# Kernel tuning notes

Measured on AMD Instinct MI355X. Metric: run time of the kernel, lower is better.

## Reference

```python
import jax, jax.numpy as jnp
import numpy as np

DIM = 192
T, H, W = 6, 8, 8
NH = 6
HD = DIM // NH
HW = H * W
N = T * HW
SCALE = HD ** (-0.5)
B_ = 128


def _sine_pos_enc():
    # Faithful port of get_sine_position_encoding(window_size[1:], dim // 2).
    npf = DIM // 2
    ones = jnp.ones((1, H, W), jnp.float32)
    y_embed = jnp.cumsum(ones, axis=1)
    x_embed = jnp.cumsum(ones, axis=2)
    two_pi = 2.0 * np.pi
    y_embed = y_embed / (y_embed[:, -1:, :] + 1e-6) * two_pi
    x_embed = x_embed / (x_embed[:, :, -1:] + 1e-6) * two_pi
    dim_t = jnp.arange(npf, dtype=jnp.float32)
    dim_t = 10000.0 ** (2.0 * jnp.floor(dim_t / 2.0) / npf)
    pos_x = x_embed[:, :, :, None] / dim_t
    pos_y = y_embed[:, :, :, None] / dim_t
    pos_x = jnp.stack((jnp.sin(pos_x[..., 0::2]), jnp.cos(pos_x[..., 1::2])), axis=4).reshape(1, H, W, npf)
    pos_y = jnp.stack((jnp.sin(pos_y[..., 0::2]), jnp.cos(pos_y[..., 1::2])), axis=4).reshape(1, H, W, npf)
    pos = jnp.concatenate((pos_y, pos_x), axis=3)  # (1, H, W, DIM)
    return pos.reshape(1, HW, DIM)


def setup_inputs() -> dict:
    key = jax.random.key(0)
    ks = jax.random.split(key, 6)
    s = 0.02
    return {
        "x": jax.random.normal(ks[0], (B_, N, DIM), jnp.float32),
        "Wqkv": jax.random.normal(ks[1], (3 * DIM, DIM), jnp.float32) * s,
        "Wproj": jax.random.normal(ks[2], (DIM, 2 * DIM), jnp.float32) * s,
        "bproj": jnp.zeros((DIM,), jnp.float32),
        "gamma": jnp.ones((DIM,), jnp.float32),
        "beta": jnp.zeros((DIM,), jnp.float32),
        "W1": jax.random.normal(ks[3], (DIM, DIM), jnp.float32) * s,
        "b1": jnp.zeros((DIM,), jnp.float32),
        "W2": jax.random.normal(ks[4], (DIM, DIM), jnp.float32) * s,
        "b2": jnp.zeros((DIM,), jnp.float32),
    }


def reference(x, Wqkv, Wproj, bproj, gamma, beta, W1, b1, W2, b2):
    b = x.shape[0]
    pos = jnp.tile(_sine_pos_enc(), (1, T, 1))  # (1, N, DIM)
    qkv = (x + pos) @ Wqkv.T                      # (b, N, 3*DIM)
    qkv = qkv.reshape(b, N, 3, NH, HD).transpose(2, 0, 3, 1, 4)
    # temporal chunks: (b, NH, T, HW, HD)
    q = qkv[0].reshape(b, NH, T, HW, HD)
    k = qkv[1].reshape(b, NH, T, HW, HD)
    v = qkv[2].reshape(b, NH, T, HW, HD)
    # all T x T cross-frame attention pairs at once
    scores = jnp.einsum('bhind,bhjmd->ijbhnm', q * SCALE, k)  # (T,T,b,NH,HW,HW)
    attn = jax.nn.softmax(scores, axis=-1)
    o = jnp.einsum('ijbhnm,bhjmd->ijbnhd', attn, v).reshape(T, T, b, HW, DIM)
    # Faithful to torch's x.view(-1, B_, HW, C): raw reinterpretation, not a transpose.
    x_tmp = x.reshape(T, b, HW, DIM)
    xi = jnp.broadcast_to(x_tmp[:, None], (T, T, b, HW, DIM))
    x_att = jnp.concatenate((o, xi), axis=-1)     # (T,T,b,HW,2*DIM)
    y = x_att @ Wproj.T + bproj
    mu = jnp.mean(y, axis=-1, keepdims=True)
    var = jnp.var(y, axis=-1, keepdims=True)
    y = (y - mu) / jnp.sqrt(var + 1e-5) * gamma + beta
    y = jax.nn.gelu(y @ W1.T + b1, approximate=False) @ W2.T + b2
    acc = jnp.sum(y, axis=1)                       # sum over j -> (T,b,HW,DIM)
    x_out = x + acc.transpose(1, 0, 2, 3).reshape(b, N, DIM) / T
    return jnp.concatenate((x, x_out), axis=-1)
```

## Files before the change

kernel.cpp:

```cpp
#include <hip/hip_runtime.h>
#include <cmath>

#define TT   6
#define NB   128
#define DIM  192
#define SCALE 0.17677669529663687f

typedef __attribute__((ext_vector_type(8))) short v8s;
typedef __attribute__((ext_vector_type(4))) float v4f;

__device__ __forceinline__ short f2bf(float f) {
  union { float f; unsigned u; } v; v.f = f;
  unsigned r = v.u + 0x7fffu + ((v.u >> 16) & 1u);
  return (short)(r >> 16);
}

__global__ void prep_kernel(const float* __restrict__ Wqkv, const float* __restrict__ Wproj,
                            const float* __restrict__ W1, const float* __restrict__ W2,
                            short* __restrict__ dWqkv, short* __restrict__ dWproj,
                            short* __restrict__ dW1, short* __restrict__ dW2,
                            float* __restrict__ pos) {
  int idx = blockIdx.x * 256 + threadIdx.x;
  const float* src = nullptr; short* dst = nullptr; int off = 0;
  if (idx < 27648)      { src = Wqkv;  dst = dWqkv;  off = idx; }
  else if (idx < 46080) { src = Wproj; dst = dWproj; off = idx - 27648; }
  else if (idx < 55296) { src = W1;    dst = dW1;    off = idx - 46080; }
  else if (idx < 64512) { src = W2;    dst = dW2;    off = idx - 55296; }
  else if (idx < 67584) {
    int p0 = (idx - 64512) * 4;
    float4 r;
    float* rp = (float*)&r;
#pragma unroll
    for (int jj = 0; jj < 4; jj++) {
      int p = p0 + jj;
      int row = p / 192, c = p - row * 192;
      int e  = (c < 96) ? (row >> 3) : (row & 7);
      int cc = (c < 96) ? c : c - 96;
      int m = cc >> 1;
      float embed = (float)(e + 1) * (6.283185307179586f / 8.000001f);
      float dt = powf(10000.0f, (float)m * (1.0f / 48.0f));
      float ang = embed / dt;
      rp[jj] = (cc & 1) ? cosf(ang) : sinf(ang);
    }
    *(float4*)(pos + p0) = r;
    return;
  } else return;
  const float* s = src + off * 4;
  short4 r;
  r.x = f2bf(s[0]); r.y = f2bf(s[1]); r.z = f2bf(s[2]); r.w = f2bf(s[3]);
  *(short4*)(dst + off * 4) = r;
}

__global__ __launch_bounds__(256) void qkv_kernel(
    const float* __restrict__ x, const float* __restrict__ pos,
    const short* __restrict__ Wqkv_bf,
    short* __restrict__ Qb, short* __restrict__ Kb, short* __restrict__ Vtb) {
  __shared__ short XP[64 * 200];
  int bid = blockIdx.x;
  int xcd = bid & 7, idx = bid >> 3;
  int bq = idx / TT;
  int b = xcd * 16 + bq, t = idx - bq * TT;
  int tid = threadIdx.x, w = tid >> 6, lane = tid & 63;
  int l15 = lane & 15, quad = lane >> 4;
  const float* xrow = x + (size_t)(b * (TT * 64) + t * 64) * DIM;
  for (int c = tid; c < 64 * 24; c += 256) {
    int row = c / 24, col8 = (c - (c / 24) * 24) * 8;
    const float* xs = xrow + row * DIM + col8;
    const float* pp = pos + row * DIM + col8;
    v8s r8;
#pragma unroll
    for (int jj = 0; jj < 8; jj++) r8[jj] = f2bf(xs[jj] + pp[jj]);
    *(v8s*)(XP + row * 200 + col8) = r8;
  }
  __syncthreads();
  const v4f vzero = {0.f, 0.f, 0.f, 0.f};
  size_t obase = (size_t)(b * TT + t) * 64 * DIM;
#pragma unroll
  for (int cti = 0; cti < 9; cti++) {
    int r0 = w * 144 + cti * 16;
    v4f acc[4] = {vzero, vzero, vzero, vzero};
#pragma unroll
    for (int ks = 0; ks < 6; ks++) {
      v8s a = *(const v8s*)(Wqkv_bf + (size_t)(r0 + l15) * 192 + ks * 32 + quad * 8);
#pragma unroll
      for (int nt = 0; nt < 4; nt++) {
        v8s bb = *(const v8s*)(XP + (nt * 16 + l15) * 200 + ks * 32 + quad * 8);
        acc[nt] = __builtin_amdgcn_mfma_f32_16x16x32_bf16(a, bb, acc[nt], 0, 0, 0);
      }
    }
    int R = r0 + quad * 4;
#pragma unroll
    for (int nt = 0; nt < 4; nt++) {
      int hw = nt * 16 + l15;
      if (R < 192) {
        short4 s;
        s.x = f2bf(acc[nt][0] * SCALE); s.y = f2bf(acc[nt][1] * SCALE);
        s.z = f2bf(acc[nt][2] * SCALE); s.w = f2bf(acc[nt][3] * SCALE);
        *(short4*)(Qb + obase + (size_t)hw * 192 + R) = s;
      } else if (R < 384) {
        short4 s;
        s.x = f2bf(acc[nt][0]); s.y = f2bf(acc[nt][1]);
        s.z = f2bf(acc[nt][2]); s.w = f2bf(acc[nt][3]);
        *(short4*)(Kb + obase + (size_t)hw * 192 + (R - 192)) = s;
      } else {
#pragma unroll
        for (int r = 0; r < 4; r++)
          Vtb[obase + (size_t)(R - 384 + r) * 64 + hw] = f2bf(acc[nt][r]);
      }
    }
  }
}

__global__ __launch_bounds__(256, 4) void fused_all(
    const float* __restrict__ x,
    const short* __restrict__ Qb, const short* __restrict__ Kb,
    const short* __restrict__ Vtb,
    const short* __restrict__ Wproj_bf, const short* __restrict__ W1_bf,
    const short* __restrict__ W2_bf,
    const float* __restrict__ bproj, const float* __restrict__ gamma,
    const float* __restrict__ beta, const float* __restrict__ b1,
    const float* __restrict__ b2,
    float* __restrict__ out) {
  __shared__ short SP[32 * 200];
  __shared__ short HB[32 * 200];
  __shared__ float LNp[32][4][2];

  int bid = blockIdx.x;
  int xcd = bid & 7, idx = bid >> 3;
  int bq = idx / 12;
  int rem = idx - bq * 12;
  int i = rem >> 1, half = rem & 1;
  int b = xcd * 16 + bq;

  int tid = threadIdx.x, w = tid >> 6, lane = tid & 63;
  int l15 = lane & 15, quad = lane >> 4;
  int wc = w;
  int qt = w & 1, hg = w >> 1;
  int cb = wc * 48;
  const v4f vzero = {0.f, 0.f, 0.f, 0.f};

  const float* xi = x + (size_t)((i * NB + b) * 64 + half * 32) * DIM;
  for (int c = tid; c < 32 * 24; c += 256) {
    int row = c / 24, col8 = (c - (c / 24) * 24) * 8;
    const float* xs = xi + row * DIM + col8;
    v8s r8;
#pragma unroll
    for (int jj = 0; jj < 8; jj++) r8[jj] = f2bf(xs[jj]);
    *(v8s*)(SP + row * 200 + col8) = r8;
  }

  const short* Qi = Qb + (size_t)(b * TT + i) * 64 * DIM;
  v8s qa[3];
#pragma unroll
  for (int hh = 0; hh < 3; hh++)
    qa[hh] = *(const v8s*)(Qi + (size_t)(half * 32 + qt * 16 + l15) * 192 + (hg * 3 + hh) * 32 + quad * 8);

  v4f acc[3][2];
#pragma unroll
  for (int cti = 0; cti < 3; cti++)
#pragma unroll
    for (int nt = 0; nt < 2; nt++) acc[cti][nt] = vzero;

  __syncthreads();

  v4f y1x[3][2];
#pragma unroll
  for (int cti = 0; cti < 3; cti++)
#pragma unroll
    for (int nt = 0; nt < 2; nt++) y1x[cti][nt] = vzero;
#pragma unroll
  for (int ks = 0; ks < 6; ks++) {
    v8s bxi[2];
#pragma unroll
    for (int nt = 0; nt < 2; nt++)
      bxi[nt] = *(const v8s*)(SP + (nt * 16 + l15) * 200 + ks * 32 + quad * 8);
#pragma unroll
    for (int cti = 0; cti < 3; cti++) {
      v8s a = *(const v8s*)(Wproj_bf + (size_t)(cb + cti * 16 + l15) * 384 + 192 + ks * 32 + quad * 8);
#pragma unroll
      for (int nt = 0; nt < 2; nt++)
        y1x[cti][nt] = __builtin_amdgcn_mfma_f32_16x16x32_bf16(a, bxi[nt], y1x[cti][nt], 0, 0, 0);
    }
  }

  int srcA = l15 + ((lane & 16) << 1);
  int srcB = srcA + 16;
  bool hiq = (lane & 32) != 0;

  for (int j = 0; j < TT; j++) {
    __syncthreads();
    {
      const short* Kj = Kb + (size_t)(b * TT + j) * 64 * DIM;
      const short* Vj = Vtb + (size_t)(b * TT + j) * 64 * DIM;
#pragma unroll
      for (int hh = 0; hh < 3; hh++) {
        int h = hg * 3 + hh;
        v4f S[4];
#pragma unroll
        for (int cta = 0; cta < 4; cta++) {
          v8s akq = *(const v8s*)(Kj + (size_t)(cta * 16 + l15) * 192 + h * 32 + quad * 8);
          S[cta] = __builtin_amdgcn_mfma_f32_16x16x32_bf16(akq, qa[hh], vzero, 0, 0, 0);
        }
        float mx = -1e30f;
#pragma unroll
        for (int cta = 0; cta < 4; cta++)
#pragma unroll
          for (int r = 0; r < 4; r++) mx = fmaxf(mx, S[cta][r]);
        mx = fmaxf(mx, __shfl_xor(mx, 16, 64));
        mx = fmaxf(mx, __shfl_xor(mx, 32, 64));
        float sum = 0.f;
#pragma unroll
        for (int cta = 0; cta < 4; cta++)
#pragma unroll
          for (int r = 0; r < 4; r++) {
            float e = __expf(S[cta][r] - mx);
            S[cta][r] = e; sum += e;
          }
        sum += __shfl_xor(sum, 16, 64);
        sum += __shfl_xor(sum, 32, 64);
        float inv = 1.0f / sum;
        unsigned pk00, pk01, pk10, pk11, pk20, pk21, pk30, pk31;
        {
          float a0 = S[0][0] * inv, a1 = S[0][1] * inv, a2 = S[0][2] * inv, a3 = S[0][3] * inv;
          __asm__("v_cvt_pk_bf16_f32 %0, %1, %2" : "=v"(pk00) : "v"(a0), "v"(a1));
          __asm__("v_cvt_pk_bf16_f32 %0, %1, %2" : "=v"(pk01) : "v"(a2), "v"(a3));
          float b0 = S[1][0] * inv, b1_ = S[1][1] * inv, b2_ = S[1][2] * inv, b3 = S[1][3] * inv;
          __asm__("v_cvt_pk_bf16_f32 %0, %1, %2" : "=v"(pk10) : "v"(b0), "v"(b1_));
          __asm__("v_cvt_pk_bf16_f32 %0, %1, %2" : "=v"(pk11) : "v"(b2_), "v"(b3));
          float c0 = S[2][0] * inv, c1 = S[2][1] * inv, c2 = S[2][2] * inv, c3 = S[2][3] * inv;
          __asm__("v_cvt_pk_bf16_f32 %0, %1, %2" : "=v"(pk20) : "v"(c0), "v"(c1));
          __asm__("v_cvt_pk_bf16_f32 %0, %1, %2" : "=v"(pk21) : "v"(c2), "v"(c3));
          float d0 = S[3][0] * inv, d1 = S[3][1] * inv, d2 = S[3][2] * inv, d3 = S[3][3] * inv;
          __asm__("v_cvt_pk_bf16_f32 %0, %1, %2" : "=v"(pk30) : "v"(d0), "v"(d1));
          __asm__("v_cvt_pk_bf16_f32 %0, %1, %2" : "=v"(pk31) : "v"(d2), "v"(d3));
        }
        union { unsigned u[4]; v8s v; } B0, B1;
        {
          unsigned ta = (unsigned)__shfl((int)pk00, srcA), tb = (unsigned)__shfl((int)pk10, srcA);
          B0.u[0] = hiq ? tb : ta;
          ta = (unsigned)__shfl((int)pk01, srcA); tb = (unsigned)__shfl((int)pk11, srcA);
          B0.u[1] = hiq ? tb : ta;
          ta = (unsigned)__shfl((int)pk00, srcB); tb = (unsigned)__shfl((int)pk10, srcB);
          B0.u[2] = hiq ? tb : ta;
          ta = (unsigned)__shfl((int)pk01, srcB); tb = (unsigned)__shfl((int)pk11, srcB);
          B0.u[3] = hiq ? tb : ta;
          ta = (unsigned)__shfl((int)pk20, srcA); tb = (unsigned)__shfl((int)pk30, srcA);
          B1.u[0] = hiq ? tb : ta;
          ta = (unsigned)__shfl((int)pk21, srcA); tb = (unsigned)__shfl((int)pk31, srcA);
          B1.u[1] = hiq ? tb : ta;
          ta = (unsigned)__shfl((int)pk20, srcB); tb = (unsigned)__shfl((int)pk30, srcB);
          B1.u[2] = hiq ? tb : ta;
          ta = (unsigned)__shfl((int)pk21, srcB); tb = (unsigned)__shfl((int)pk31, srcB);
          B1.u[3] = hiq ? tb : ta;
        }
#pragma unroll
        for (int ct2 = 0; ct2 < 2; ct2++) {
          v8s av0 = *(const v8s*)(Vj + (size_t)(h * 32 + ct2 * 16 + l15) * 64 + quad * 8);
          v8s av1 = *(const v8s*)(Vj + (size_t)(h * 32 + ct2 * 16 + l15) * 64 + 32 + quad * 8);
          v4f o = __builtin_amdgcn_mfma_f32_16x16x32_bf16(av0, B0.v, vzero, 0, 0, 0);
          o = __builtin_amdgcn_mfma_f32_16x16x32_bf16(av1, B1.v, o, 0, 0, 0);
          short4 s;
          s.x = f2bf(o[0]); s.y = f2bf(o[1]); s.z = f2bf(o[2]); s.w = f2bf(o[3]);
          *(short4*)(&SP[(qt * 16 + l15) * 200 + h * 32 + ct2 * 16 + quad * 4]) = s;
        }
      }
    }
    __syncthreads();

    v4f y1[3][2];
#pragma unroll
    for (int cti = 0; cti < 3; cti++)
#pragma unroll
      for (int nt = 0; nt < 2; nt++) y1[cti][nt] = y1x[cti][nt];
#pragma unroll
    for (int ks = 0; ks < 6; ks++) {
      v8s bo[2];
#pragma unroll
      for (int nt = 0; nt < 2; nt++)
        bo[nt] = *(const v8s*)(SP + (nt * 16 + l15) * 200 + ks * 32 + quad * 8);
#pragma unroll
      for (int cti = 0; cti < 3; cti++) {
        v8s a = *(const v8s*)(Wproj_bf + (size_t)(cb + cti * 16 + l15) * 384 + ks * 32 + quad * 8);
#pragma unroll
        for (int nt = 0; nt < 2; nt++)
          y1[cti][nt] = __builtin_amdgcn_mfma_f32_16x16x32_bf16(a, bo[nt], y1[cti][nt], 0, 0, 0);
      }
    }
#pragma unroll
    for (int cti = 0; cti < 3; cti++) {
      float4 bp4 = *(const float4*)(bproj + cb + cti * 16 + quad * 4);
#pragma unroll
      for (int nt = 0; nt < 2; nt++) {
        y1[cti][nt][0] += bp4.x; y1[cti][nt][1] += bp4.y;
        y1[cti][nt][2] += bp4.z; y1[cti][nt][3] += bp4.w;
      }
    }
#pragma unroll
    for (int nt = 0; nt < 2; nt++) {
      float s1 = 0.f, s2 = 0.f;
#pragma unroll
      for (int cti = 0; cti < 3; cti++)
#pragma unroll
        for (int r = 0; r < 4; r++) { float v = y1[cti][nt][r]; s1 += v; s2 += v * v; }
      s1 += __shfl_xor(s1, 16, 64); s2 += __shfl_xor(s2, 16, 64);
      s1 += __shfl_xor(s1, 32, 64); s2 += __shfl_xor(s2, 32, 64);
      if (quad == 0) {
        LNp[nt * 16 + l15][wc][0] = s1;
        LNp[nt * 16 + l15][wc][1] = s2;
      }
    }
    __syncthreads();
    float mu[2], rs[2];
#pragma unroll
    for (int nt = 0; nt < 2; nt++) {
      int row = nt * 16 + l15;
      float s1 = 0.f, s2 = 0.f;
#pragma unroll
      for (int ww = 0; ww < 4; ww++) { s1 += LNp[row][ww][0]; s2 += LNp[row][ww][1]; }
      float m = s1 * (1.0f / 192.0f);
      mu[nt] = m; rs[nt] = rsqrtf(s2 * (1.0f / 192.0f) - m * m + 1e-5f);
    }
#pragma unroll
    for (int cti = 0; cti < 3; cti++) {
      float4 g4 = *(const float4*)(gamma + cb + cti * 16 + quad * 4);
      float4 be4 = *(const float4*)(beta + cb + cti * 16 + quad * 4);
#pragma unroll
      for (int nt = 0; nt < 2; nt++) {
        short4 s;
        s.x = f2bf((y1[cti][nt][0] - mu[nt]) * rs[nt] * g4.x + be4.x);
        s.y = f2bf((y1[cti][nt][1] - mu[nt]) * rs[nt] * g4.y + be4.y);
        s.z = f2bf((y1[cti][nt][2] - mu[nt]) * rs[nt] * g4.z + be4.z);
        s.w = f2bf((y1[cti][nt][3] - mu[nt]) * rs[nt] * g4.w + be4.w);
        *(short4*)(&SP[(nt * 16 + l15) * 200 + cb + cti * 16 + quad * 4]) = s;
      }
    }
    __syncthreads();

    v4f y2[3][2];
#pragma unroll
    for (int cti = 0; cti < 3; cti++)
#pragma unroll
      for (int nt = 0; nt < 2; nt++) y2[cti][nt] = vzero;
#pragma unroll
    for (int ks = 0; ks < 6; ks++) {
      v8s bh[2];
#pragma unroll
      for (int nt = 0; nt < 2; nt++)
        bh[nt] = *(const v8s*)(SP + (nt * 16 + l15) * 200 + ks * 32 + quad * 8);
#pragma unroll
      for (int cti = 0; cti < 3; cti++) {
        v8s a = *(const v8s*)(W1_bf + (size_t)(cb + cti * 16 + l15) * 192 + ks * 32 + quad * 8);
#pragma unroll
        for (int nt = 0; nt < 2; nt++)
          y2[cti][nt] = __builtin_amdgcn_mfma_f32_16x16x32_bf16(a, bh[nt], y2[cti][nt], 0, 0, 0);
      }
    }
#pragma unroll
    for (int cti = 0; cti < 3; cti++) {
      float4 b14 = *(const float4*)(b1 + cb + cti * 16 + quad * 4);
#pragma unroll
      for (int nt = 0; nt < 2; nt++) {
        float vv[4] = {y2[cti][nt][0] + b14.x, y2[cti][nt][1] + b14.y,
                       y2[cti][nt][2] + b14.z, y2[cti][nt][3] + b14.w};
        short sv[4];
#pragma unroll
        for (int r = 0; r < 4; r++) {
          float v = vv[r];
          float t = 0.79788456080286536f * (v + 0.044715f * v * v * v);
          float e = __expf(2.0f * t);
          float th = 1.0f - 2.0f / (e + 1.0f);
          sv[r] = f2bf(0.5f * v * (1.0f + th));
        }
        short4 s;
        s.x = sv[0]; s.y = sv[1]; s.z = sv[2]; s.w = sv[3];
        *(short4*)(&HB[(nt * 16 + l15) * 200 + cb + cti * 16 + quad * 4]) = s;
      }
    }
    __syncthreads();

#pragma unroll
    for (int ks = 0; ks < 6; ks++) {
      v8s bh[2];
#pragma unroll
      for (int nt = 0; nt < 2; nt++)
        bh[nt] = *(const v8s*)(HB + (nt * 16 + l15) * 200 + ks * 32 + quad * 8);
#pragma unroll
      for (int cti = 0; cti < 3; cti++) {
        v8s a = *(const v8s*)(W2_bf + (size_t)(cb + cti * 16 + l15) * 192 + ks * 32 + quad * 8);
#pragma unroll
        for (int nt = 0; nt < 2; nt++)
          acc[cti][nt] = __builtin_amdgcn_mfma_f32_16x16x32_bf16(a, bh[nt], acc[cti][nt], 0, 0, 0);
      }
    }
  }

  float* SPf = (float*)SP;
#pragma unroll
  for (int pass = 0; pass < 2; pass++) {
    __syncthreads();
#pragma unroll
    for (int cti = 0; cti < 3; cti++) {
      float4 o4;
      o4.x = acc[cti][pass][0] * (1.0f / 6.0f);
      o4.y = acc[cti][pass][1] * (1.0f / 6.0f);
      o4.z = acc[cti][pass][2] * (1.0f / 6.0f);
      o4.w = acc[cti][pass][3] * (1.0f / 6.0f);
      *(float4*)(&SPf[l15 * 196 + cb + cti * 16 + quad * 4]) = o4;
    }
    __syncthreads();
    for (int c = tid; c < 768; c += 256) {
      int r16 = c / 48, col4 = (c - r16 * 48) * 4;
      int row = half * 32 + pass * 16 + r16;
      size_t nrow = (size_t)b * 384 + (size_t)i * 64 + row;
      float4 xv = *(const float4*)(x + nrow * DIM + col4);
      float4 b24 = *(const float4*)(b2 + col4);
      float4 av = *(const float4*)(&SPf[r16 * 196 + col4]);
      float4 o4;
      o4.x = xv.x + av.x + b24.x;
      o4.y = xv.y + av.y + b24.y;
      o4.z = xv.z + av.z + b24.z;
      o4.w = xv.w + av.w + b24.w;
      *(float4*)(out + nrow * 384 + col4) = xv;
      *(float4*)(out + nrow * 384 + 192 + col4) = o4;
    }
  }
}

extern "C" void kernel_launch(void* const* d_in, const int* in_sizes, int n_in,
                              void* d_out, int out_size, void* d_ws, size_t ws_size,
                              hipStream_t stream) {
  (void)in_sizes; (void)n_in; (void)out_size; (void)ws_size;
  const float* x     = (const float*)d_in[0];
  const float* Wqkv  = (const float*)d_in[1];
  const float* Wproj = (const float*)d_in[2];
  const float* bproj = (const float*)d_in[3];
  const float* gamma = (const float*)d_in[4];
  const float* beta  = (const float*)d_in[5];
  const float* W1    = (const float*)d_in[6];
  const float* b1    = (const float*)d_in[7];
  const float* W2    = (const float*)d_in[8];
  const float* b2    = (const float*)d_in[9];
  float* out = (float*)d_out;

  short* Wqkv_bf  = (short*)d_ws;
  short* Wproj_bf = Wqkv_bf + 110592;
  short* W1_bf    = Wproj_bf + 73728;
  short* W2_bf    = W1_bf + 36864;
  float* pos_f    = (float*)(W2_bf + 36864);
  short* Qb       = (short*)(pos_f + 12288);
  short* Kb       = Qb + 9437184;
  short* Vtb      = Kb + 9437184;

  prep_kernel<<<dim3(264), dim3(256), 0, stream>>>(
      Wqkv, Wproj, W1, W2, Wqkv_bf, Wproj_bf, W1_bf, W2_bf, pos_f);
  qkv_kernel<<<dim3(TT * NB), dim3(256), 0, stream>>>(x, pos_f, Wqkv_bf, Qb, Kb, Vtb);
  fused_all<<<dim3(TT * NB * 2), dim3(256), 0, stream>>>(
      x, Qb, Kb, Vtb, Wproj_bf, W1_bf, W2_bf, bproj, gamma, beta, b1, b2, out);
}
```

Before: 561.8 us.

## Prefetch next GEMM weights into registers with double-buffered fragment sets

After: 567.0 us. No clear change (+0.9%).

```diff
diff --git a/kernel.cpp b/kernel.cpp
--- a/kernel.cpp
+++ b/kernel.cpp
@@ -13,6 +13,12 @@
   union { float f; unsigned u; } v; v.f = f;
   unsigned r = v.u + 0x7fffu + ((v.u >> 16) & 1u);
   return (short)(r >> 16);
+}
+
+__device__ __forceinline__ void ldsbar() {
+  __asm__ volatile("s_waitcnt lgkmcnt(0)" ::: "memory");
+  __builtin_amdgcn_s_barrier();
+  __asm__ volatile("" ::: "memory");
 }
 
 __global__ void prep_kernel(const float* __restrict__ Wqkv, const float* __restrict__ Wproj,
@@ -111,7 +117,232 @@
   }
 }
 
-__global__ __launch_bounds__(256, 4) void fused_all(
+__device__ __forceinline__ void ptrans(const v4f S[4], float inv,
+                                       int srcA, int srcB, bool hiq,
+                                       v8s& B0v, v8s& B1v) {
+  unsigned pk00, pk01, pk10, pk11, pk20, pk21, pk30, pk31;
+  {
+    float a0 = S[0][0] * inv, a1 = S[0][1] * inv, a2 = S[0][2] * inv, a3 = S[0][3] * inv;
+    __asm__("v_cvt_pk_bf16_f32 %0, %1, %2" : "=v"(pk00) : "v"(a0), "v"(a1));
+    __asm__("v_cvt_pk_bf16_f32 %0, %1, %2" : "=v"(pk01) : "v"(a2), "v"(a3));
+    float b0 = S[1][0] * inv, b1_ = S[1][1] * inv, b2_ = S[1][2] * inv, b3 = S[1][3] * inv;
+    __asm__("v_cvt_pk_bf16_f32 %0, %1, %2" : "=v"(pk10) : "v"(b0), "v"(b1_));
+    __asm__("v_cvt_pk_bf16_f32 %0, %1, %2" : "=v"(pk11) : "v"(b2_), "v"(b3));
+    float c0 = S[2][0] * inv, c1 = S[2][1] * inv, c2 = S[2][2] * inv, c3 = S[2][3] * inv;
+    __asm__("v_cvt_pk_bf16_f32 %0, %1, %2" : "=v"(pk20) : "v"(c0), "v"(c1));
+    __asm__("v_cvt_pk_bf16_f32 %0, %1, %2" : "=v"(pk21) : "v"(c2), "v"(c3));
+    float d0 = S[3][0] * inv, d1 = S[3][1] * inv, d2 = S[3][2] * inv, d3 = S[3][3] * inv;
+    __asm__("v_cvt_pk_bf16_f32 %0, %1, %2" : "=v"(pk30) : "v"(d0), "v"(d1));
+    __asm__("v_cvt_pk_bf16_f32 %0, %1, %2" : "=v"(pk31) : "v"(d2), "v"(d3));
+  }
+  union { unsigned u[4]; v8s v; } B0, B1;
+  unsigned ta, tb;
+  ta = (unsigned)__shfl((int)pk00, srcA); tb = (unsigned)__shfl((int)pk10, srcA);
+  B0.u[0] = hiq ? tb : ta;
+  ta = (unsigned)__shfl((int)pk01, srcA); tb = (unsigned)__shfl((int)pk11, srcA);
+  B0.u[1] = hiq ? tb : ta;
+  ta = (unsigned)__shfl((int)pk00, srcB); tb = (unsigned)__shfl((int)pk10, srcB);
+  B0.u[2] = hiq ? tb : ta;
+  ta = (unsigned)__shfl((int)pk01, srcB); tb = (unsigned)__shfl((int)pk11, srcB);
+  B0.u[3] = hiq ? tb : ta;
+  ta = (unsigned)__shfl((int)pk20, srcA); tb = (unsigned)__shfl((int)pk30, srcA);
+  B1.u[0] = hiq ? tb : ta;
+  ta = (unsigned)__shfl((int)pk21, srcA); tb = (unsigned)__shfl((int)pk31, srcA);
+  B1.u[1] = hiq ? tb : ta;
+  ta = (unsigned)__shfl((int)pk20, srcB); tb = (unsigned)__shfl((int)pk30, srcB);
+  B1.u[2] = hiq ? tb : ta;
+  ta = (unsigned)__shfl((int)pk21, srcB); tb = (unsigned)__shfl((int)pk31, srcB);
+  B1.u[3] = hiq ? tb : ta;
+  B0v = B0.v; B1v = B1.v;
+}
+
+__device__ __forceinline__ void issue_w(v8s (&dst)[6][3], const short* __restrict__ Wp,
+                                        int rstride, int coff, int rbase, int quad) {
+#pragma unroll
+  for (int ks = 0; ks < 6; ks++)
+#pragma unroll
+    for (int cti = 0; cti < 3; cti++)
+      dst[ks][cti] = *(const v8s*)(Wp + (size_t)(rbase + cti * 16) * rstride + coff + ks * 32 + quad * 8);
+}
+
+__device__ __forceinline__ void gemm_consume(const v8s (&wu)[6][3], v4f (&yy)[3][2],
+                                             const short* __restrict__ SRC, int l15, int quad) {
+#pragma unroll
+  for (int ks = 0; ks < 6; ks++) {
+    v8s b0 = *(const v8s*)(SRC + (size_t)(l15) * 200 + ks * 32 + quad * 8);
+    v8s b1 = *(const v8s*)(SRC + (size_t)(16 + l15) * 200 + ks * 32 + quad * 8);
+#pragma unroll
+    for (int cti = 0; cti < 3; cti++) {
+      yy[cti][0] = __builtin_amdgcn_mfma_f32_16x16x32_bf16(wu[ks][cti], b0, yy[cti][0], 0, 0, 0);
+      yy[cti][1] = __builtin_amdgcn_mfma_f32_16x16x32_bf16(wu[ks][cti], b1, yy[cti][1], 0, 0, 0);
+    }
+  }
+}
+
+__device__ __forceinline__ void attn_phase(const short* __restrict__ Kj,
+                                           const short* __restrict__ Vj,
+                                           const v8s (&qa)[3], short* __restrict__ SP,
+                                           int l15, int quad, int hg, int qt,
+                                           int srcA, int srcB, bool hiq) {
+  const v4f vzero = {0.f, 0.f, 0.f, 0.f};
+#pragma unroll
+  for (int hh = 0; hh < 3; hh++) {
+    int h = hg * 3 + hh;
+    v8s kf[4];
+#pragma unroll
+    for (int cta = 0; cta < 4; cta++)
+      kf[cta] = *(const v8s*)(Kj + (size_t)(cta * 16 + l15) * 192 + h * 32 + quad * 8);
+    v4f S[4];
+#pragma unroll
+    for (int cta = 0; cta < 4; cta++)
+      S[cta] = __builtin_amdgcn_mfma_f32_16x16x32_bf16(kf[cta], qa[hh], vzero, 0, 0, 0);
+    v8s vf0a = *(const v8s*)(Vj + (size_t)(h * 32 + l15) * 64 + quad * 8);
+    v8s vf0b = *(const v8s*)(Vj + (size_t)(h * 32 + l15) * 64 + 32 + quad * 8);
+    v8s vf1a = *(const v8s*)(Vj + (size_t)(h * 32 + 16 + l15) * 64 + quad * 8);
+    v8s vf1b = *(const v8s*)(Vj + (size_t)(h * 32 + 16 + l15) * 64 + 32 + quad * 8);
+    float mx = -1e30f;
+#pragma unroll
+    for (int cta = 0; cta < 4; cta++)
+#pragma unroll
+      for (int r = 0; r < 4; r++) mx = fmaxf(mx, S[cta][r]);
+    mx = fmaxf(mx, __shfl_xor(mx, 16, 64));
+    mx = fmaxf(mx, __shfl_xor(mx, 32, 64));
+    float sum = 0.f;
+#pragma unroll
+    for (int cta = 0; cta < 4; cta++)
+#pragma unroll
+      for (int r = 0; r < 4; r++) {
+        float e = __expf(S[cta][r] - mx);
+        S[cta][r] = e; sum += e;
+      }
+    sum += __shfl_xor(sum, 16, 64);
+    sum += __shfl_xor(sum, 32, 64);
+    float inv = 1.0f / sum;
+    v8s B0, B1;
+    ptrans(S, inv, srcA, srcB, hiq, B0, B1);
+    v4f o0 = __builtin_amdgcn_mfma_f32_16x16x32_bf16(vf0a, B0, vzero, 0, 0, 0);
+    o0 = __builtin_amdgcn_mfma_f32_16x16x32_bf16(vf0b, B1, o0, 0, 0, 0);
+    short4 s0;
+    s0.x = f2bf(o0[0]); s0.y = f2bf(o0[1]); s0.z = f2bf(o0[2]); s0.w = f2bf(o0[3]);
+    *(short4*)(&SP[(qt * 16 + l15) * 200 + h * 32 + quad * 4]) = s0;
+    v4f o1 = __builtin_amdgcn_mfma_f32_16x16x32_bf16(vf1a, B0, vzero, 0, 0, 0);
+    o1 = __builtin_amdgcn_mfma_f32_16x16x32_bf16(vf1b, B1, o1, 0, 0, 0);
+    short4 s1;
+    s1.x = f2bf(o1[0]); s1.y = f2bf(o1[1]); s1.z = f2bf(o1[2]); s1.w = f2bf(o1[3]);
+    *(short4*)(&SP[(qt * 16 + l15) * 200 + h * 32 + 16 + quad * 4]) = s1;
+  }
+}
+
+__device__ __forceinline__ void ln_reduce_store(v4f (&y1)[3][2], const float* __restrict__ bproj,
+                                                float (*LNp)[4][2], int cb, int l15, int quad, int wc) {
+#pragma unroll
+  for (int cti = 0; cti < 3; cti++) {
+    float4 bp4 = *(const float4*)(bproj + cb + cti * 16 + quad * 4);
+#pragma unroll
+    for (int nt = 0; nt < 2; nt++) {
+      y1[cti][nt][0] += bp4.x; y1[cti][nt][1] += bp4.y;
+      y1[cti][nt][2] += bp4.z; y1[cti][nt][3] += bp4.w;
+    }
+  }
+#pragma unroll
+  for (int nt = 0; nt < 2; nt++) {
+    float s1 = 0.f, s2 = 0.f;
+#pragma unroll
+    for (int cti = 0; cti < 3; cti++)
+#pragma unroll
+      for (int r = 0; r < 4; r++) { float v = y1[cti][nt][r]; s1 += v; s2 += v * v; }
+    s1 += __shfl_xor(s1, 16, 64); s2 += __shfl_xor(s2, 16, 64);
+    s1 += __shfl_xor(s1, 32, 64); s2 += __shfl_xor(s2, 32, 64);
+    if (quad == 0) { LNp[nt * 16 + l15][wc][0] = s1; LNp[nt * 16 + l15][wc][1] = s2; }
+  }
+}
+
+__device__ __forceinline__ void ln_normalize_store(const v4f (&y1)[3][2],
+                                                   const float* __restrict__ gamma,
+                                                   const float* __restrict__ beta,
+                                                   const float (*LNp)[4][2],
+                                                   short* __restrict__ SP,
+                                                   int cb, int l15, int quad) {
+  float mu[2], rs[2];
+#pragma unroll
+  for (int nt = 0; nt < 2; nt++) {
+    int row = nt * 16 + l15;
+    float s1 = 0.f, s2 = 0.f;
+#pragma unroll
+    for (int ww = 0; ww < 4; ww++) { s1 += LNp[row][ww][0]; s2 += LNp[row][ww][1]; }
+    float m = s1 * (1.0f / 192.0f);
+    mu[nt] = m; rs[nt] = rsqrtf(s2 * (1.0f / 192.0f) - m * m + 1e-5f);
+  }
+#pragma unroll
+  for (int cti = 0; cti < 3; cti++) {
+    float4 g4 = *(const float4*)(gamma + cb + cti * 16 + quad * 4);
+    float4 be4 = *(const float4*)(beta + cb + cti * 16 + quad * 4);
+#pragma unroll
+    for (int nt = 0; nt < 2; nt++) {
+      short4 s;
+      s.x = f2bf((y1[cti][nt][0] - mu[nt]) * rs[nt] * g4.x + be4.x);
+      s.y = f2bf((y1[cti][nt][1] - mu[nt]) * rs[nt] * g4.y + be4.y);
+      s.z = f2bf((y1[cti][nt][2] - mu[nt]) * rs[nt] * g4.z + be4.z);
+      s.w = f2bf((y1[cti][nt][3] - mu[nt]) * rs[nt] * g4.w + be4.w);
+      *(short4*)(&SP[(nt * 16 + l15) * 200 + cb + cti * 16 + quad * 4]) = s;
+    }
+  }
+}
+
+__device__ __forceinline__ void gelu_store(const v4f (&y2)[3][2], const float* __restrict__ b1,
+                                           short* __restrict__ HB, int cb, int l15, int quad) {
+#pragma unroll
+  for (int cti = 0; cti < 3; cti++) {
+    float4 b14 = *(const float4*)(b1 + cb + cti * 16 + quad * 4);
+#pragma unroll
+    for (int nt = 0; nt < 2; nt++) {
+      float vv[4] = {y2[cti][nt][0] + b14.x, y2[cti][nt][1] + b14.y,
+                     y2[cti][nt][2] + b14.z, y2[cti][nt][3] + b14.w};
+      short sv[4];
+#pragma unroll
+      for (int r = 0; r < 4; r++) {
+        float v = vv[r];
+        float t = 0.79788456080286536f * (v + 0.044715f * v * v * v);
+        float e = __expf(2.0f * t);
+        float th = 1.0f - 2.0f / (e + 1.0f);
+        sv[r] = f2bf(0.5f * v * (1.0f + th));
+      }
+      short4 s;
+      s.x = sv[0]; s.y = sv[1]; s.z = sv[2]; s.w = sv[3];
+      *(short4*)(&HB[(nt * 16 + l15) * 200 + cb + cti * 16 + quad * 4]) = s;
+    }
+  }
+}
+
+#define JBODY(WU, WN, JV)                                                      \
+  {                                                                            \
+    int j = (JV);                                                              \
+    ldsbar();                      \
+    attn_phase(Kb + (size_t)(b * TT + j) * 64 * DIM,                           \
+               Vtb + (size_t)(b * TT + j) * 64 * DIM,                          \
+               qa, SP, l15, quad, hg, qt, srcA, srcB, hiq);                    \
+    ldsbar();                                                  \
+    v4f y1[3][2];                                                              \
+    _Pragma("unroll") for (int c_ = 0; c_ < 3; c_++)                           \
+      _Pragma("unroll") for (int n_ = 0; n_ < 2; n_++) y1[c_][n_] = y1x[c_][n_]; \
+    gemm_consume(WU, y1, SP, l15, quad);                                       \
+    issue_w(WN, W1_bf, 192, 0, cb + l15, quad);                                \
+    ln_reduce_store(y1, bproj, LNp, cb, l15, quad, wc);                        \
+    ldsbar();                       \
+    ln_normalize_store(y1, gamma, beta, LNp, SP, cb, l15, quad);               \
+    ldsbar();                                                \
+    v4f y2[3][2];                                                              \
+    _Pragma("unroll") for (int c_ = 0; c_ < 3; c_++)                           \
+      _Pragma("unroll") for (int n_ = 0; n_ < 2; n_++) y2[c_][n_] = vzero;     \
+    gemm_consume(WN, y2, SP, l15, quad);                                       \
+    issue_w(WU, W2_bf, 192, 0, cb + l15, quad);                                \
+    gelu_store(y2, b1, HB, cb, l15, quad);                                     \
+    ldsbar();                                \
+    gemm_consume(WU, acc, HB, l15, quad);                                      \
+    if (j < TT - 1) issue_w(WN, Wproj_bf, 384, 0, cb + l15, quad);             \
+  }
+
+__global__ __launch_bounds__(256, 2) void fused_all(
     const float* __restrict__ x,
     const short* __restrict__ Qb, const short* __restrict__ Kb,
     const short* __restrict__ Vtb,
@@ -161,7 +392,7 @@
 #pragma unroll
     for (int nt = 0; nt < 2; nt++) acc[cti][nt] = vzero;
 
-  __syncthreads();
+  ldsbar();
 
   v4f y1x[3][2];
 #pragma unroll
@@ -170,16 +401,13 @@
     for (int nt = 0; nt < 2; nt++) y1x[cti][nt] = vzero;
 #pragma unroll
   for (int ks = 0; ks < 6; ks++) {
-    v8s bxi[2];
-#pragma unroll
-    for (int nt = 0; nt < 2; nt++)
-      bxi[nt] = *(const v8s*)(SP + (nt * 16 + l15) * 200 + ks * 32 + quad * 8);
+    v8s bxi0 = *(const v8s*)(SP + (size_t)(l15) * 200 + ks * 32 + quad * 8);
+    v8s bxi1 = *(const v8s*)(SP + (size_t)(16 + l15) * 200 + ks * 32 + quad * 8);
 #pragma unroll
     for (int cti = 0; cti < 3; cti++) {
       v8s a = *(const v8s*)(Wproj_bf + (size_t)(cb + cti * 16 + l15) * 384 + 192 + ks * 32 + quad * 8);
-#pragma unroll
-      for (int nt = 0; nt < 2; nt++)
-        y1x[cti][nt] = __builtin_amdgcn_mfma_f32_16x16x32_bf16(a, bxi[nt], y1x[cti][nt], 0, 0, 0);
+      y1x[cti][0] = __builtin_amdgcn_mfma_f32_16x16x32_bf16(a, bxi0, y1x[cti][0], 0, 0, 0);
+      y1x[cti][1] = __builtin_amdgcn_mfma_f32_16x16x32_bf16(a, bxi1, y1x[cti][1], 0, 0, 0);
     }
   }
 
@@ -187,217 +415,18 @@
   int srcB = srcA + 16;
   bool hiq = (lane & 32) != 0;
 
-  for (int j = 0; j < TT; j++) {
-    __syncthreads();
-    {
-      const short* Kj = Kb + (size_t)(b * TT + j) * 64 * DIM;
-      const short* Vj = Vtb + (size_t)(b * TT + j) * 64 * DIM;
-#pragma unroll
-      for (int hh = 0; hh < 3; hh++) {
-        int h = hg * 3 + hh;
-        v4f S[4];
-#pragma unroll
-        for (int cta = 0; cta < 4; cta++) {
-          v8s akq = *(const v8s*)(Kj + (size_t)(cta * 16 + l15) * 192 + h * 32 + quad * 8);
-          S[cta] = __builtin_amdgcn_mfma_f32_16x16x32_bf16(akq, qa[hh], vzero, 0, 0, 0);
-        }
-        float mx = -1e30f;
-#pragma unroll
-        for (int cta = 0; cta < 4; cta++)
-#pragma unroll
-          for (int r = 0; r < 4; r++) mx = fmaxf(mx, S[cta][r]);
-        mx = fmaxf(mx, __shfl_xor(mx, 16, 64));
-        mx = fmaxf(mx, __shfl_xor(mx, 32, 64));
-        float sum = 0.f;
-#pragma unroll
-        for (int cta = 0; cta < 4; cta++)
-#pragma unroll
-          for (int r = 0; r < 4; r++) {
-            float e = __expf(S[cta][r] - mx);
-            S[cta][r] = e; sum += e;
-          }
-        sum += __shfl_xor(sum, 16, 64);
-        sum += __shfl_xor(sum, 32, 64);
-        float inv = 1.0f / sum;
-        unsigned pk00, pk01, pk10, pk11, pk20, pk21, pk30, pk31;
-        {
-          float a0 = S[0][0] * inv, a1 = S[0][1] * inv, a2 = S[0][2] * inv, a3 = S[0][3] * inv;
-          __asm__("v_cvt_pk_bf16_f32 %0, %1, %2" : "=v"(pk00) : "v"(a0), "v"(a1));
-          __asm__("v_cvt_pk_bf16_f32 %0, %1, %2" : "=v"(pk01) : "v"(a2), "v"(a3));
-          float b0 = S[1][0] * inv, b1_ = S[1][1] * inv, b2_ = S[1][2] * inv, b3 = S[1][3] * inv;
-          __asm__("v_cvt_pk_bf16_f32 %0, %1, %2" : "=v"(pk10) : "v"(b0), "v"(b1_));
-          __asm__("v_cvt_pk_bf16_f32 %0, %1, %2" : "=v"(pk11) : "v"(b2_), "v"(b3));
-          float c0 = S[2][0] * inv, c1 = S[2][1] * inv, c2 = S[2][2] * inv, c3 = S[2][3] * inv;
-          __asm__("v_cvt_pk_bf16_f32 %0, %1, %2" : "=v"(pk20) : "v"(c0), "v"(c1));
-          __asm__("v_cvt_pk_bf16_f32 %0, %1, %2" : "=v"(pk21) : "v"(c2), "v"(c3));
-          float d0 = S[3][0] * inv, d1 = S[3][1] * inv, d2 = S[3][2] * inv, d3 = S[3][3] * inv;
-          __asm__("v_cvt_pk_bf16_f32 %0, %1, %2" : "=v"(pk30) : "v"(d0), "v"(d1));
-          __asm__("v_cvt_pk_bf16_f32 %0, %1, %2" : "=v"(pk31) : "v"(d2), "v"(d3));
-        }
-        union { unsigned u[4]; v8s v; } B0, B1;
-        {
-          unsigned ta = (unsigned)__shfl((int)pk00, srcA), tb = (unsigned)__shfl((int)pk10, srcA);
-          B0.u[0] = hiq ? tb : ta;
-          ta = (unsigned)__shfl((int)pk01, srcA); tb = (unsigned)__shfl((int)pk11, srcA);
-          B0.u[1] = hiq ? tb : ta;
-          ta = (unsigned)__shfl((int)pk00, srcB); tb = (unsigned)__shfl((int)pk10, srcB);
-          B0.u[2] = hiq ? tb : ta;
-          ta = (unsigned)__shfl((int)pk01, srcB); tb = (unsigned)__shfl((int)pk11, srcB);
-          B0.u[3] = hiq ? tb : ta;
-          ta = (unsigned)__shfl((int)pk20, srcA); tb = (unsigned)__shfl((int)pk30, srcA);
-          B1.u[0] = hiq ? tb : ta;
-          ta = (unsigned)__shfl((int)pk21, srcA); tb = (unsigned)__shfl((int)pk31, srcA);
-          B1.u[1] = hiq ? tb : ta;
-          ta = (unsigned)__shfl((int)pk20, srcB); tb = (unsigned)__shfl((int)pk30, srcB);
-          B1.u[2] = hiq ? tb : ta;
-          ta = (unsigned)__shfl((int)pk21, srcB); tb = (unsigned)__shfl((int)pk31, srcB);
-          B1.u[3] = hiq ? tb : ta;
-        }
-#pragma unroll
-        for (int ct2 = 0; ct2 < 2; ct2++) {
-          v8s av0 = *(const v8s*)(Vj + (size_t)(h * 32 + ct2 * 16 + l15) * 64 + quad * 8);
-          v8s av1 = *(const v8s*)(Vj + (size_t)(h * 32 + ct2 * 16 + l15) * 64 + 32 + quad * 8);
-          v4f o = __builtin_amdgcn_mfma_f32_16x16x32_bf16(av0, B0.v, vzero, 0, 0, 0);
-          o = __builtin_amdgcn_mfma_f32_16x16x32_bf16(av1, B1.v, o, 0, 0, 0);
-          short4 s;
-          s.x = f2bf(o[0]); s.y = f2bf(o[1]); s.z = f2bf(o[2]); s.w = f2bf(o[3]);
-          *(short4*)(&SP[(qt * 16 + l15) * 200 + h * 32 + ct2 * 16 + quad * 4]) = s;
-        }
-      }
-    }
-    __syncthreads();
-
-    v4f y1[3][2];
-#pragma unroll
-    for (int cti = 0; cti < 3; cti++)
-#pragma unroll
-      for (int nt = 0; nt < 2; nt++) y1[cti][nt] = y1x[cti][nt];
-#pragma unroll
-    for (int ks = 0; ks < 6; ks++) {
-      v8s bo[2];
-#pragma unroll
-      for (int nt = 0; nt < 2; nt++)
-        bo[nt] = *(const v8s*)(SP + (nt * 16 + l15) * 200 + ks * 32 + quad * 8);
-#pragma unroll
-      for (int cti = 0; cti < 3; cti++) {
-        v8s a = *(const v8s*)(Wproj_bf + (size_t)(cb + cti * 16 + l15) * 384 + ks * 32 + quad * 8);
-#pragma unroll
-        for (int nt = 0; nt < 2; nt++)
-          y1[cti][nt] = __builtin_amdgcn_mfma_f32_16x16x32_bf16(a, bo[nt], y1[cti][nt], 0, 0, 0);
-      }
-    }
-#pragma unroll
-    for (int cti = 0; cti < 3; cti++) {
-      float4 bp4 = *(const float4*)(bproj + cb + cti * 16 + quad * 4);
-#pragma unroll
-      for (int nt = 0; nt < 2; nt++) {
-        y1[cti][nt][0] += bp4.x; y1[cti][nt][1] += bp4.y;
-        y1[cti][nt][2] += bp4.z; y1[cti][nt][3] += bp4.w;
-      }
-    }
-#pragma unroll
-    for (int nt = 0; nt < 2; nt++) {
-      float s1 = 0.f, s2 = 0.f;
-#pragma unroll
-      for (int cti = 0; cti < 3; cti++)
-#pragma unroll
-        for (int r = 0; r < 4; r++) { float v = y1[cti][nt][r]; s1 += v; s2 += v * v; }
-      s1 += __shfl_xor(s1, 16, 64); s2 += __shfl_xor(s2, 16, 64);
-      s1 += __shfl_xor(s1, 32, 64); s2 += __shfl_xor(s2, 32, 64);
-      if (quad == 0) {
-        LNp[nt * 16 + l15][wc][0] = s1;
-        LNp[nt * 16 + l15][wc][1] = s2;
-      }
-    }
-    __syncthreads();
-    float mu[2], rs[2];
-#pragma unroll
-    for (int nt = 0; nt < 2; nt++) {
-      int row = nt * 16 + l15;
-      float s1 = 0.f, s2 = 0.f;
-#pragma unroll
-      for (int ww = 0; ww < 4; ww++) { s1 += LNp[row][ww][0]; s2 += LNp[row][ww][1]; }
-      float m = s1 * (1.0f / 192.0f);
-      mu[nt] = m; rs[nt] = rsqrtf(s2 * (1.0f / 192.0f) - m * m + 1e-5f);
-    }
-#pragma unroll
-    for (int cti = 0; cti < 3; cti++) {
-      float4 g4 = *(const float4*)(gamma + cb + cti * 16 + quad * 4);
-      float4 be4 = *(const float4*)(beta + cb + cti * 16 + quad * 4);
-#pragma unroll
-      for (int nt = 0; nt < 2; nt++) {
-        short4 s;
-        s.x = f2bf((y1[cti][nt][0] - mu[nt]) * rs[nt] * g4.x + be4.x);
-        s.y = f2bf((y1[cti][nt][1] - mu[nt]) * rs[nt] * g4.y + be4.y);
-        s.z = f2bf((y1[cti][nt][2] - mu[nt]) * rs[nt] * g4.z + be4.z);
-        s.w = f2bf((y1[cti][nt][3] - mu[nt]) * rs[nt] * g4.w + be4.w);
-        *(short4*)(&SP[(nt * 16 + l15) * 200 + cb + cti * 16 + quad * 4]) = s;
-      }
-    }
-    __syncthreads();
-
-    v4f y2[3][2];
-#pragma unroll
-    for (int cti = 0; cti < 3; cti++)
-#pragma unroll
-      for (int nt = 0; nt < 2; nt++) y2[cti][nt] = vzero;
-#pragma unroll
-    for (int ks = 0; ks < 6; ks++) {
-      v8s bh[2];
-#pragma unroll
-      for (int nt = 0; nt < 2; nt++)
-        bh[nt] = *(const v8s*)(SP + (nt * 16 + l15) * 200 + ks * 32 + quad * 8);
-#pragma unroll
-      for (int cti = 0; cti < 3; cti++) {
-        v8s a = *(const v8s*)(W1_bf + (size_t)(cb + cti * 16 + l15) * 192 + ks * 32 + quad * 8);
-#pragma unroll
-        for (int nt = 0; nt < 2; nt++)
-          y2[cti][nt] = __builtin_amdgcn_mfma_f32_16x16x32_bf16(a, bh[nt], y2[cti][nt], 0, 0, 0);
-      }
-    }
-#pragma unroll
-    for (int cti = 0; cti < 3; cti++) {
-      float4 b14 = *(const float4*)(b1 + cb + cti * 16 + quad * 4);
-#pragma unroll
-      for (int nt = 0; nt < 2; nt++) {
-        float vv[4] = {y2[cti][nt][0] + b14.x, y2[cti][nt][1] + b14.y,
-                       y2[cti][nt][2] + b14.z, y2[cti][nt][3] + b14.w};
-        short sv[4];
-#pragma unroll
-        for (int r = 0; r < 4; r++) {
-          float v = vv[r];
-          float t = 0.79788456080286536f * (v + 0.044715f * v * v * v);
-          float e = __expf(2.0f * t);
-          float th = 1.0f - 2.0f / (e + 1.0f);
-          sv[r] = f2bf(0.5f * v * (1.0f + th));
-        }
-        short4 s;
-        s.x = sv[0]; s.y = sv[1]; s.z = sv[2]; s.w = sv[3];
-        *(short4*)(&HB[(nt * 16 + l15) * 200 + cb + cti * 16 + quad * 4]) = s;
-      }
-    }
-    __syncthreads();
-
-#pragma unroll
-    for (int ks = 0; ks < 6; ks++) {
-      v8s bh[2];
-#pragma unroll
-      for (int nt = 0; nt < 2; nt++)
-        bh[nt] = *(const v8s*)(HB + (nt * 16 + l15) * 200 + ks * 32 + quad * 8);
-#pragma unroll
-      for (int cti = 0; cti < 3; cti++) {
-        v8s a = *(const v8s*)(W2_bf + (size_t)(cb + cti * 16 + l15) * 192 + ks * 32 + quad * 8);
-#pragma unroll
-        for (int nt = 0; nt < 2; nt++)
-          acc[cti][nt] = __builtin_amdgcn_mfma_f32_16x16x32_bf16(a, bh[nt], acc[cti][nt], 0, 0, 0);
-      }
-    }
+  v8s wA[6][3], wB[6][3];
+  issue_w(wA, Wproj_bf, 384, 0, cb + l15, quad);
+
+  for (int jp = 0; jp < 3; jp++) {
+    JBODY(wA, wB, jp * 2);
+    JBODY(wB, wA, jp * 2 + 1);
   }
 
   float* SPf = (float*)SP;
 #pragma unroll
   for (int pass = 0; pass < 2; pass++) {
-    __syncthreads();
+    ldsbar();
 #pragma unroll
     for (int cti = 0; cti < 3; cti++) {
       float4 o4;
@@ -407,7 +436,7 @@
       o4.w = acc[cti][pass][3] * (1.0f / 6.0f);
       *(float4*)(&SPf[l15 * 196 + cb + cti * 16 + quad * 4]) = o4;
     }
-    __syncthreads();
+    ldsbar();
     for (int c = tid; c < 768; c += 256) {
       int r16 = c / 48, col4 = (c - r16 * 48) * 4;
       int row = half * 32 + pass * 16 + r16;
```

## Recompute x-projection per frame to cut register pressure and prefetch K/V fragments

Applied to the files above, without the earlier changes.

After: 717.1 us. 1.28x slower.

```diff
diff --git a/kernel.cpp b/kernel.cpp
--- a/kernel.cpp
+++ b/kernel.cpp
@@ -111,6 +111,45 @@
   }
 }
 
+__device__ __forceinline__ void ptrans(const v4f S[4], float inv,
+                                       int srcA, int srcB, bool hiq,
+                                       v8s& B0v, v8s& B1v) {
+  unsigned pk00, pk01, pk10, pk11, pk20, pk21, pk30, pk31;
+  {
+    float a0 = S[0][0] * inv, a1 = S[0][1] * inv, a2 = S[0][2] * inv, a3 = S[0][3] * inv;
+    __asm__("v_cvt_pk_bf16_f32 %0, %1, %2" : "=v"(pk00) : "v"(a0), "v"(a1));
+    __asm__("v_cvt_pk_bf16_f32 %0, %1, %2" : "=v"(pk01) : "v"(a2), "v"(a3));
+    float b0 = S[1][0] * inv, b1_ = S[1][1] * inv, b2_ = S[1][2] * inv, b3 = S[1][3] * inv;
+    __asm__("v_cvt_pk_bf16_f32 %0, %1, %2" : "=v"(pk10) : "v"(b0), "v"(b1_));
+    __asm__("v_cvt_pk_bf16_f32 %0, %1, %2" : "=v"(pk11) : "v"(b2_), "v"(b3));
+    float c0 = S[2][0] * inv, c1 = S[2][1] * inv, c2 = S[2][2] * inv, c3 = S[2][3] * inv;
+    __asm__("v_cvt_pk_bf16_f32 %0, %1, %2" : "=v"(pk20) : "v"(c0), "v"(c1));
+    __asm__("v_cvt_pk_bf16_f32 %0, %1, %2" : "=v"(pk21) : "v"(c2), "v"(c3));
+    float d0 = S[3][0] * inv, d1 = S[3][1] * inv, d2 = S[3][2] * inv, d3 = S[3][3] * inv;
+    __asm__("v_cvt_pk_bf16_f32 %0, %1, %2" : "=v"(pk30) : "v"(d0), "v"(d1));
+    __asm__("v_cvt_pk_bf16_f32 %0, %1, %2" : "=v"(pk31) : "v"(d2), "v"(d3));
+  }
+  union { unsigned u[4]; v8s v; } B0, B1;
+  unsigned ta, tb;
+  ta = (unsigned)__shfl((int)pk00, srcA); tb = (unsigned)__shfl((int)pk10, srcA);
+  B0.u[0] = hiq ? tb : ta;
+  ta = (unsigned)__shfl((int)pk01, srcA); tb = (unsigned)__shfl((int)pk11, srcA);
+  B0.u[1] = hiq ? tb : ta;
+  ta = (unsigned)__shfl((int)pk00, srcB); tb = (unsigned)__shfl((int)pk10, srcB);
+  B0.u[2] = hiq ? tb : ta;
+  ta = (unsigned)__shfl((int)pk01, srcB); tb = (unsigned)__shfl((int)pk11, srcB);
+  B0.u[3] = hiq ? tb : ta;
+  ta = (unsigned)__shfl((int)pk20, srcA); tb = (unsigned)__shfl((int)pk30, srcA);
+  B1.u[0] = hiq ? tb : ta;
+  ta = (unsigned)__shfl((int)pk21, srcA); tb = (unsigned)__shfl((int)pk31, srcA);
+  B1.u[1] = hiq ? tb : ta;
+  ta = (unsigned)__shfl((int)pk20, srcB); tb = (unsigned)__shfl((int)pk30, srcB);
+  B1.u[2] = hiq ? tb : ta;
+  ta = (unsigned)__shfl((int)pk21, srcB); tb = (unsigned)__shfl((int)pk31, srcB);
+  B1.u[3] = hiq ? tb : ta;
+  B0v = B0.v; B1v = B1.v;
+}
+
 __global__ __launch_bounds__(256, 4) void fused_all(
     const float* __restrict__ x,
     const short* __restrict__ Qb, const short* __restrict__ Kb,
@@ -139,54 +178,22 @@
   int cb = wc * 48;
   const v4f vzero = {0.f, 0.f, 0.f, 0.f};
 
-  const float* xi = x + (size_t)((i * NB + b) * 64 + half * 32) * DIM;
-  for (int c = tid; c < 32 * 24; c += 256) {
-    int row = c / 24, col8 = (c - (c / 24) * 24) * 8;
-    const float* xs = xi + row * DIM + col8;
-    v8s r8;
-#pragma unroll
-    for (int jj = 0; jj < 8; jj++) r8[jj] = f2bf(xs[jj]);
-    *(v8s*)(SP + row * 200 + col8) = r8;
-  }
-
   const short* Qi = Qb + (size_t)(b * TT + i) * 64 * DIM;
-  v8s qa[3];
-#pragma unroll
-  for (int hh = 0; hh < 3; hh++)
-    qa[hh] = *(const v8s*)(Qi + (size_t)(half * 32 + qt * 16 + l15) * 192 + (hg * 3 + hh) * 32 + quad * 8);
+  int qrow = half * 32 + qt * 16 + l15;
 
   v4f acc[3][2];
 #pragma unroll
   for (int cti = 0; cti < 3; cti++)
 #pragma unroll
     for (int nt = 0; nt < 2; nt++) acc[cti][nt] = vzero;
-
-  __syncthreads();
-
-  v4f y1x[3][2];
-#pragma unroll
-  for (int cti = 0; cti < 3; cti++)
-#pragma unroll
-    for (int nt = 0; nt < 2; nt++) y1x[cti][nt] = vzero;
-#pragma unroll
-  for (int ks = 0; ks < 6; ks++) {
-    v8s bxi[2];
-#pragma unroll
-    for (int nt = 0; nt < 2; nt++)
-      bxi[nt] = *(const v8s*)(SP + (nt * 16 + l15) * 200 + ks * 32 + quad * 8);
-#pragma unroll
-    for (int cti = 0; cti < 3; cti++) {
-      v8s a = *(const v8s*)(Wproj_bf + (size_t)(cb + cti * 16 + l15) * 384 + 192 + ks * 32 + quad * 8);
-#pragma unroll
-      for (int nt = 0; nt < 2; nt++)
-        y1x[cti][nt] = __builtin_amdgcn_mfma_f32_16x16x32_bf16(a, bxi[nt], y1x[cti][nt], 0, 0, 0);
-    }
-  }
 
   int srcA = l15 + ((lane & 16) << 1);
   int srcB = srcA + 16;
   bool hiq = (lane & 32) != 0;
 
+  const float* xr0 = x + ((size_t)(i * NB + b) * 64 + half * 32 + l15) * DIM;
+  const float* xr1 = xr0 + 16 * DIM;
+
   for (int j = 0; j < TT; j++) {
     __syncthreads();
     {
@@ -195,12 +202,19 @@
 #pragma unroll
       for (int hh = 0; hh < 3; hh++) {
         int h = hg * 3 + hh;
+        v8s qa = *(const v8s*)(Qi + (size_t)qrow * 192 + h * 32 + quad * 8);
+        v8s kf[4];
+#pragma unroll
+        for (int cta = 0; cta < 4; cta++)
+          kf[cta] = *(const v8s*)(Kj + (size_t)(cta * 16 + l15) * 192 + h * 32 + quad * 8);
         v4f S[4];
 #pragma unroll
-        for (int cta = 0; cta < 4; cta++) {
-          v8s akq = *(const v8s*)(Kj + (size_t)(cta * 16 + l15) * 192 + h * 32 + quad * 8);
-          S[cta] = __builtin_amdgcn_mfma_f32_16x16x32_bf16(akq, qa[hh], vzero, 0, 0, 0);
-        }
+        for (int cta = 0; cta < 4; cta++)
+          S[cta] = __builtin_amdgcn_mfma_f32_16x16x32_bf16(kf[cta], qa, vzero, 0, 0, 0);
+        v8s vf0a = *(const v8s*)(Vj + (size_t)(h * 32 + l15) * 64 + quad * 8);
+        v8s vf0b = *(const v8s*)(Vj + (size_t)(h * 32 + l15) * 64 + 32 + quad * 8);
+        v8s vf1a = *(const v8s*)(Vj + (size_t)(h * 32 + 16 + l15) * 64 + quad * 8);
+        v8s vf1b = *(const v8s*)(Vj + (size_t)(h * 32 + 16 + l15) * 64 + 32 + quad * 8);
         float mx = -1e30f;
 #pragma unroll
         for (int cta = 0; cta < 4; cta++)
@@ -219,50 +233,18 @@
         sum += __shfl_xor(sum, 16, 64);
         sum += __shfl_xor(sum, 32, 64);
         float inv = 1.0f / sum;
-        unsigned pk00, pk01, pk10, pk11, pk20, pk21, pk30, pk31;
-        {
-          float a0 = S[0][0] * inv, a1 = S[0][1] * inv, a2 = S[0][2] * inv, a3 = S[0][3] * inv;
-          __asm__("v_cvt_pk_bf16_f32 %0, %1, %2" : "=v"(pk00) : "v"(a0), "v"(a1));
-          __asm__("v_cvt_pk_bf16_f32 %0, %1, %2" : "=v"(pk01) : "v"(a2), "v"(a3));
-          float b0 = S[1][0] * inv, b1_ = S[1][1] * inv, b2_ = S[1][2] * inv, b3 = S[1][3] * inv;
-          __asm__("v_cvt_pk_bf16_f32 %0, %1, %2" : "=v"(pk10) : "v"(b0), "v"(b1_));
-          __asm__("v_cvt_pk_bf16_f32 %0, %1, %2" : "=v"(pk11) : "v"(b2_), "v"(b3));
-          float c0 = S[2][0] * inv, c1 = S[2][1] * inv, c2 = S[2][2] * inv, c3 = S[2][3] * inv;
-          __asm__("v_cvt_pk_bf16_f32 %0, %1, %2" : "=v"(pk20) : "v"(c0), "v"(c1));
-          __asm__("v_cvt_pk_bf16_f32 %0, %1, %2" : "=v"(pk21) : "v"(c2), "v"(c3));
-          float d0 = S[3][0] * inv, d1 = S[3][1] * inv, d2 = S[3][2] * inv, d3 = S[3][3] * inv;
-          __asm__("v_cvt_pk_bf16_f32 %0, %1, %2" : "=v"(pk30) : "v"(d0), "v"(d1));
-          __asm__("v_cvt_pk_bf16_f32 %0, %1, %2" : "=v"(pk31) : "v"(d2), "v"(d3));
-        }
-        union { unsigned u[4]; v8s v; } B0, B1;
-        {
-          unsigned ta = (unsigned)__shfl((int)pk00, srcA), tb = (unsigned)__shfl((int)pk10, srcA);
-          B0.u[0] = hiq ? tb : ta;
-          ta = (unsigned)__shfl((int)pk01, srcA); tb = (unsigned)__shfl((int)pk11, srcA);
-          B0.u[1] = hiq ? tb : ta;
-          ta = (unsigned)__shfl((int)pk00, srcB); tb = (unsigned)__shfl((int)pk10, srcB);
-          B0.u[2] = hiq ? tb : ta;
-          ta = (unsigned)__shfl((int)pk01, srcB); tb = (unsigned)__shfl((int)pk11, srcB);
-          B0.u[3] = hiq ? tb : ta;
-          ta = (unsigned)__shfl((int)pk20, srcA); tb = (unsigned)__shfl((int)pk30, srcA);
-          B1.u[0] = hiq ? tb : ta;
-          ta = (unsigned)__shfl((int)pk21, srcA); tb = (unsigned)__shfl((int)pk31, srcA);
-          B1.u[1] = hiq ? tb : ta;
-          ta = (unsigned)__shfl((int)pk20, srcB); tb = (unsigned)__shfl((int)pk30, srcB);
-          B1.u[2] = hiq ? tb : ta;
-          ta = (unsigned)__shfl((int)pk21, srcB); tb = (unsigned)__shfl((int)pk31, srcB);
-          B1.u[3] = hiq ? tb : ta;
-        }
-#pragma unroll
-        for (int ct2 = 0; ct2 < 2; ct2++) {
-          v8s av0 = *(const v8s*)(Vj + (size_t)(h * 32 + ct2 * 16 + l15) * 64 + quad * 8);
-          v8s av1 = *(const v8s*)(Vj + (size_t)(h * 32 + ct2 * 16 + l15) * 64 + 32 + quad * 8);
-          v4f o = __builtin_amdgcn_mfma_f32_16x16x32_bf16(av0, B0.v, vzero, 0, 0, 0);
-          o = __builtin_amdgcn_mfma_f32_16x16x32_bf16(av1, B1.v, o, 0, 0, 0);
-          short4 s;
-          s.x = f2bf(o[0]); s.y = f2bf(o[1]); s.z = f2bf(o[2]); s.w = f2bf(o[3]);
-          *(short4*)(&SP[(qt * 16 + l15) * 200 + h * 32 + ct2 * 16 + quad * 4]) = s;
-        }
+        v8s B0, B1;
+        ptrans(S, inv, srcA, srcB, hiq, B0, B1);
+        v4f o0 = __builtin_amdgcn_mfma_f32_16x16x32_bf16(vf0a, B0, vzero, 0, 0, 0);
+        o0 = __builtin_amdgcn_mfma_f32_16x16x32_bf16(vf0b, B1, o0, 0, 0, 0);
+        short4 s0;
+        s0.x = f2bf(o0[0]); s0.y = f2bf(o0[1]); s0.z = f2bf(o0[2]); s0.w = f2bf(o0[3]);
+        *(short4*)(&SP[(qt * 16 + l15) * 200 + h * 32 + quad * 4]) = s0;
+        v4f o1 = __builtin_amdgcn_mfma_f32_16x16x32_bf16(vf1a, B0, vzero, 0, 0, 0);
+        o1 = __builtin_amdgcn_mfma_f32_16x16x32_bf16(vf1b, B1, o1, 0, 0, 0);
+        short4 s1;
+        s1.x = f2bf(o1[0]); s1.y = f2bf(o1[1]); s1.z = f2bf(o1[2]); s1.w = f2bf(o1[3]);
+        *(short4*)(&SP[(qt * 16 + l15) * 200 + h * 32 + 16 + quad * 4]) = s1;
       }
     }
     __syncthreads();
@@ -271,7 +253,7 @@
 #pragma unroll
     for (int cti = 0; cti < 3; cti++)
 #pragma unroll
-      for (int nt = 0; nt < 2; nt++) y1[cti][nt] = y1x[cti][nt];
+      for (int nt = 0; nt < 2; nt++) y1[cti][nt] = vzero;
 #pragma unroll
     for (int ks = 0; ks < 6; ks++) {
       v8s bo[2];
@@ -284,6 +266,24 @@
 #pragma unroll
         for (int nt = 0; nt < 2; nt++)
           y1[cti][nt] = __builtin_amdgcn_mfma_f32_16x16x32_bf16(a, bo[nt], y1[cti][nt], 0, 0, 0);
+      }
+    }
+#pragma unroll
+    for (int ks = 0; ks < 6; ks++) {
+      v8s bx0, bx1;
+      {
+        const float* p0 = xr0 + ks * 32 + quad * 8;
+        const float* p1 = xr1 + ks * 32 + quad * 8;
+        v8s r0, r1;
+#pragma unroll
+        for (int e = 0; e < 8; e++) { r0[e] = f2bf(p0[e]); r1[e] = f2bf(p1[e]); }
+        bx0 = r0; bx1 = r1;
+      }
+#pragma unroll
+      for (int cti = 0; cti < 3; cti++) {
+        v8s a = *(const v8s*)(Wproj_bf + (size_t)(cb + cti * 16 + l15) * 384 + 192 + ks * 32 + quad * 8);
+        y1[cti][0] = __builtin_amdgcn_mfma_f32_16x16x32_bf16(a, bx0, y1[cti][0], 0, 0, 0);
+        y1[cti][1] = __builtin_amdgcn_mfma_f32_16x16x32_bf16(a, bx1, y1[cti][1], 0, 0, 0);
       }
     }
 #pragma unroll
```
